# Kernel optimization log

Measured on AMD Instinct MI355X. Metric: run time of the kernel, lower is better.

The kernel has to match this reference:

```python
import jax, jax.numpy as jnp
import numpy as np

A = 1.0          # jacobi a
B = 1.0          # jacobi b
BASE_ALPHA = 2.0
K = 10           # polynomial order
N = 16384        # nodes
C = 32           # channels


def setup_inputs() -> dict:
    key = jax.random.key(0)
    k1, k2 = jax.random.split(key, 2)
    x = jax.random.normal(k1, (N, C), dtype=jnp.float32)
    # dense graph operator (stand-in for a normalized laplacian); scaled so spectrum is O(1)
    L = jax.random.normal(k2, (N, N), dtype=jnp.float32) / np.float32(np.sqrt(N))
    conv_params = jnp.full((K + 1,), min(1.0 / BASE_ALPHA, 1.0), dtype=jnp.float32)
    comb_params = jnp.ones((K + 1, C), dtype=jnp.float32)
    return {"x": x, "L": L, "conv_params": conv_params, "comb_params": comb_params}


def reference(x, L, conv_params, comb_params):
    a, b = A, B
    alpha = BASE_ALPHA * jnp.tanh(conv_params)  # [K+1] learned step sizes
    polys = [x]  # P_0 = x
    if K >= 1:
        # with l=-1, r=1: (r+l)/(r-l)=0, 1/(r-l)=0.5
        c1 = alpha[0] * (a - b) / 2.0
        c2 = alpha[0] * (a + b + 2.0) / 2.0
        polys.append(c1 * x + c2 * (L @ x))
    for i in range(2, K + 1):
        div = 2.0 * i * (i + a + b) * (2.0 * i + a + b - 2.0)
        r1 = (2.0 * i + a + b) * (2.0 * i + a + b - 1.0) * (2.0 * i + a + b - 2.0) / div
        r2 = (2.0 * i + a + b - 1.0) * (a * a - b * b) / div
        r3 = 2.0 * (i + a - 1.0) * (i + b - 1.0) * (2.0 * i + a + b) / div
        c1 = alpha[i - 1] * r1                      # multiplies L @ P_{i-1} (coef1, since 2/(r-l)=1)
        c2 = alpha[i - 1] * r2                      # coef2 (the (r+l)/(r-l) term vanishes)
        c3 = alpha[i - 1] * alpha[i - 2] * r3       # coef_3
        polys.append(c1 * (L @ polys[-1]) + c2 * polys[-1] - c3 * polys[-2])
    # y = sum_k comb[k] (broadcast over nodes) * P_k  -- avoids materializing the stacked [K+1,N,C]
    y = polys[0] * comb_params[0][None, :]
    for k in range(1, K + 1):
        y = y + comb_params[k][None, :] * polys[k]
    return y
```

## Files before the change

### kernel.cpp

```cpp
#include <hip/hip_runtime.h>
#include <math.h>


#define NN 16384
#define CC 32
#define KPOLY 10
#define NSPLIT 16
#define KSEG (NN / NSPLIT)
#define STEPS (KSEG / 32)
#define NTK (NN / 32)

typedef _Float16 half8 __attribute__((ext_vector_type(8)));
typedef float f32x4 __attribute__((ext_vector_type(4)));
typedef unsigned int u32x4 __attribute__((ext_vector_type(4)));
typedef unsigned int u32x2 __attribute__((ext_vector_type(2)));

union U16 {
  u32x4 u;
  half8 h;
};
union H4 {
  _Float16 h[4];
  u32x2 u;
};

__global__ __launch_bounds__(256) void conv_pack_gemm1(const float* __restrict__ L,
                                                       _Float16* __restrict__ Lf,
                                                       const _Float16* __restrict__ Ph,
                                                       float* __restrict__ part) {
  __shared__ __align__(16) _Float16 lds[16 * 1024];
  const int tid = threadIdx.x;
  const int tr = blockIdx.x >> 4;
  const int sc = blockIdx.x & 15;
  const float* src = L + (size_t)tr * 16 * NN + (size_t)sc * 1024;

#pragma unroll
  for (int j = 0; j < 16; ++j) {
    const int flat = j * 256 + tid;
    const int r = flat >> 8;
    const int cu = flat & 255;
    f32x4 v = __builtin_nontemporal_load(
        reinterpret_cast<const f32x4*>(src + (size_t)r * NN) + cu);
    H4 o;
    o.h[0] = (_Float16)v.x;
    o.h[1] = (_Float16)v.y;
    o.h[2] = (_Float16)v.z;
    o.h[3] = (_Float16)v.w;
    const int u = (cu >> 1) ^ (r & 7);
    *reinterpret_cast<u32x2*>(&lds[r * 1024 + u * 8 + (cu & 1) * 4]) = o.u;
  }
  __syncthreads();

  const int lane = tid & 63;
  const int wave = tid >> 6;
  const int r = lane & 15;
  const int lg = lane >> 4;

  f32x4 acc0 = (f32x4){0.f, 0.f, 0.f, 0.f};
  f32x4 acc1 = (f32x4){0.f, 0.f, 0.f, 0.f};
#pragma unroll
  for (int i = 0; i < 8; ++i) {
    const int tkl = wave * 8 + i;
    const int u = (tkl * 4 + lg) ^ (r & 7);
    U16 aval;
    aval.u = *reinterpret_cast<const u32x4*>(&lds[r * 1024 + u * 8]);
    const size_t tk = (size_t)sc * 32 + tkl;
    __builtin_nontemporal_store(
        aval.u, reinterpret_cast<u32x4*>(Lf + ((size_t)tr * NTK + tk) * 512) + lane);
    const int kb = sc * 128 + tkl * 4 + lg;
    U16 b0, b1;
    b0.u = *reinterpret_cast<const u32x4*>(Ph + (size_t)kb * 256 + (size_t)r * 8);
    b1.u = *reinterpret_cast<const u32x4*>(Ph + (size_t)kb * 256 + (size_t)(16 + r) * 8);
    acc0 = __builtin_amdgcn_mfma_f32_16x16x32_f16(aval.h, b0.h, acc0, 0, 0, 0);
    acc1 = __builtin_amdgcn_mfma_f32_16x16x32_f16(aval.h, b1.h, acc1, 0, 0, 0);
  }
  __syncthreads();

  float* red = reinterpret_cast<float*>(lds);
#pragma unroll
  for (int j = 0; j < 4; ++j) {
    red[wave * 512 + (lg * 4 + j) * 32 + r] = acc0[j];
    red[wave * 512 + (lg * 4 + j) * 32 + 16 + r] = acc1[j];
  }
  __syncthreads();

  const int e = tid * 2;
  float2 s0 = *reinterpret_cast<const float2*>(&red[e]);
  float2 s1 = *reinterpret_cast<const float2*>(&red[512 + e]);
  float2 s2 = *reinterpret_cast<const float2*>(&red[1024 + e]);
  float2 s3 = *reinterpret_cast<const float2*>(&red[1536 + e]);
  float2 s = make_float2(s0.x + s1.x + s2.x + s3.x, s0.y + s1.y + s2.y + s3.y);
  *reinterpret_cast<float2*>(part + (size_t)sc * NN * CC + (size_t)tr * 16 * CC + e) = s;
}

__global__ __launch_bounds__(256, 4) void gemm_f16(const _Float16* __restrict__ Lf,
                                                   const _Float16* __restrict__ Ph,
                                                   float* __restrict__ part) {
  const int tid = threadIdx.x;
  const int lane = tid & 63;
  const int wave = tid >> 6;
  const int rg = blockIdx.x & 63;
  const int split = blockIdx.x >> 6;
  const int rb = rg * 256 + wave * 64;
  const int k0 = split * KSEG;
  const int tk0 = k0 >> 5;
  const int l15 = lane & 15;
  const int lg = lane >> 4;

  const u32x4* Ap[4];
#pragma unroll
  for (int rt = 0; rt < 4; ++rt)
    Ap[rt] = reinterpret_cast<const u32x4*>(
                 Lf + ((size_t)((rb >> 4) + rt) * NTK + tk0) * 512) +
             lane;
  const u32x4* Bp[2];
#pragma unroll
  for (int ct = 0; ct < 2; ++ct)
    Bp[ct] = reinterpret_cast<const u32x4*>(Ph + (size_t)(k0 / 8 + lg) * 256 +
                                            (size_t)(ct * 16 + l15) * 8);

  f32x4 acc[4][2];
#pragma unroll
  for (int rt = 0; rt < 4; ++rt)
#pragma unroll
    for (int ct = 0; ct < 2; ++ct) acc[rt][ct] = (f32x4){0.f, 0.f, 0.f, 0.f};

  U16 A[2][4], B[2][2];
#pragma unroll
  for (int rt = 0; rt < 4; ++rt) A[0][rt].u = __builtin_nontemporal_load(Ap[rt]);
#pragma unroll
  for (int ct = 0; ct < 2; ++ct) B[0][ct].u = *Bp[ct];

#pragma unroll
  for (int kk = 0; kk < STEPS; ++kk) {
    const int cur = kk & 1;
    const int nxt = cur ^ 1;
    if (kk < STEPS - 1) {
#pragma unroll
      for (int rt = 0; rt < 4; ++rt)
        A[nxt][rt].u = __builtin_nontemporal_load(Ap[rt] + (kk + 1) * 64);
#pragma unroll
      for (int ct = 0; ct < 2; ++ct)
        B[nxt][ct].u = *reinterpret_cast<const u32x4*>(
            reinterpret_cast<const _Float16*>(Bp[ct]) + 1024 * (kk + 1));
    }
#pragma unroll
    for (int rt = 0; rt < 4; ++rt)
#pragma unroll
      for (int ct = 0; ct < 2; ++ct)
        acc[rt][ct] = __builtin_amdgcn_mfma_f32_16x16x32_f16(A[cur][rt].h, B[cur][ct].h,
                                                             acc[rt][ct], 0, 0, 0);
  }

  float* pb = part + (size_t)split * NN * CC;
#pragma unroll
  for (int rt = 0; rt < 4; ++rt)
#pragma unroll
    for (int ct = 0; ct < 2; ++ct)
#pragma unroll
      for (int j = 0; j < 4; ++j)
        pb[(size_t)(rb + rt * 16 + lg * 4 + j) * CC + ct * 16 + l15] = acc[rt][ct][j];
}

__global__ __launch_bounds__(256) void init_kernel(const float* __restrict__ x,
                                                   const float* __restrict__ comb,
                                                   float* __restrict__ y,
                                                   _Float16* __restrict__ Ph) {
  int idx = blockIdx.x * blockDim.x + threadIdx.x;
  float4 xv = reinterpret_cast<const float4*>(x)[idx];
  int c4 = (idx & 7) << 2;
  int n = idx >> 3;
  float4 cb = *reinterpret_cast<const float4*>(comb + c4);
  reinterpret_cast<float4*>(y)[idx] =
      make_float4(xv.x * cb.x, xv.y * cb.y, xv.z * cb.z, xv.w * cb.w);
  size_t pb = (size_t)(n >> 3) * 256 + (size_t)c4 * 8 + (n & 7);
  Ph[pb] = (_Float16)xv.x;
  Ph[pb + 8] = (_Float16)xv.y;
  Ph[pb + 16] = (_Float16)xv.z;
  Ph[pb + 24] = (_Float16)xv.w;
}

__global__ __launch_bounds__(256) void poly_update(
    const float* __restrict__ part, float* __restrict__ Pnew,
    const float* __restrict__ Pprev, const float* __restrict__ Pprev2,
    float* __restrict__ y, _Float16* __restrict__ Ph, const float* __restrict__ conv,
    const float* __restrict__ comb_row, float r1, float r2, float r3, int ia, int ib,
    int has2) {
  int idx = blockIdx.x * blockDim.x + threadIdx.x;
  float a1 = 2.f * tanhf(conv[ia]);
  float cL = a1 * r1;
  float cP = a1 * r2;

  float4 t = make_float4(0.f, 0.f, 0.f, 0.f);
#pragma unroll
  for (int s = 0; s < NSPLIT; ++s) {
    float4 p = reinterpret_cast<const float4*>(part)[(size_t)s * (NN * CC / 4) + idx];
    t.x += p.x;
    t.y += p.y;
    t.z += p.z;
    t.w += p.w;
  }

  float4 pp = reinterpret_cast<const float4*>(Pprev)[idx];
  float4 pn;
  pn.x = cL * t.x + cP * pp.x;
  pn.y = cL * t.y + cP * pp.y;
  pn.z = cL * t.z + cP * pp.z;
  pn.w = cL * t.w + cP * pp.w;
  if (has2) {
    float a2 = 2.f * tanhf(conv[ib]);
    float cPP = a1 * a2 * r3;
    float4 p2 = reinterpret_cast<const float4*>(Pprev2)[idx];
    pn.x -= cPP * p2.x;
    pn.y -= cPP * p2.y;
    pn.z -= cPP * p2.z;
    pn.w -= cPP * p2.w;
  }
  reinterpret_cast<float4*>(Pnew)[idx] = pn;

  int c4 = (idx & 7) << 2;
  int n = idx >> 3;
  size_t pb = (size_t)(n >> 3) * 256 + (size_t)c4 * 8 + (n & 7);
  Ph[pb] = (_Float16)pn.x;
  Ph[pb + 8] = (_Float16)pn.y;
  Ph[pb + 16] = (_Float16)pn.z;
  Ph[pb + 24] = (_Float16)pn.w;

  float4 cb = *reinterpret_cast<const float4*>(comb_row + c4);
  float4 yv = reinterpret_cast<float4*>(y)[idx];
  yv.x = fmaf(cb.x, pn.x, yv.x);
  yv.y = fmaf(cb.y, pn.y, yv.y);
  yv.z = fmaf(cb.z, pn.z, yv.z);
  yv.w = fmaf(cb.w, pn.w, yv.w);
  reinterpret_cast<float4*>(y)[idx] = yv;
}

static void jacobi_r(int i, double a, double b, float& r1, float& r2, float& r3) {
  double div = 2.0 * i * (i + a + b) * (2.0 * i + a + b - 2.0);
  r1 = (float)((2.0 * i + a + b) * (2.0 * i + a + b - 1.0) * (2.0 * i + a + b - 2.0) / div);
  r2 = (float)((2.0 * i + a + b - 1.0) * (a * a - b * b) / div);
  r3 = (float)(2.0 * (i + a - 1.0) * (i + b - 1.0) * (2.0 * i + a + b) / div);
}

extern "C" void kernel_launch(void* const* d_in, const int* in_sizes, int n_in,
                              void* d_out, int out_size, void* d_ws, size_t ws_size,
                              hipStream_t stream) {
  const float* x = (const float*)d_in[0];
  const float* Lm = (const float*)d_in[1];
  const float* conv = (const float*)d_in[2];
  const float* comb = (const float*)d_in[3];
  float* y = (float*)d_out;
  char* ws = (char*)d_ws;

  _Float16* Lf = (_Float16*)ws;
  float* part = (float*)(ws + 536870912ull);
  _Float16* Ph = (_Float16*)(ws + 536870912ull + 33554432ull);
  float* Pb0 = (float*)(ws + 536870912ull + 33554432ull + 2097152ull);
  float* Pb1 = Pb0 + (size_t)NN * CC;
  float* Pb2 = Pb1 + (size_t)NN * CC;
  float* bufs[3] = {Pb0, Pb1, Pb2};

  const double Aj = 1.0, Bj = 1.0;
  const int ew_blocks = NN * CC / 4 / 256;

  init_kernel<<<ew_blocks, 256, 0, stream>>>(x, comb, y, Ph);
  conv_pack_gemm1<<<16384, 256, 0, stream>>>(Lm, Lf, Ph, part);

  const float* Pprev = x;
  const float* Pprev2 = x;
  for (int i = 1; i <= KPOLY; ++i) {
    if (i > 1) gemm_f16<<<64 * NSPLIT, 256, 0, stream>>>(Lf, Ph, part);

    float r1, r2, r3;
    if (i == 1) {
      r1 = (float)((Aj + Bj + 2.0) / 2.0);
      r2 = (float)((Aj - Bj) / 2.0);
      r3 = 0.f;
    } else {
      jacobi_r(i, Aj, Bj, r1, r2, r3);
    }
    float* Pn = bufs[(i - 1) % 3];
    poly_update<<<ew_blocks, 256, 0, stream>>>(part, Pn, Pprev, Pprev2, y, Ph, conv,
                                               comb + (size_t)i * CC, r1, r2, r3, i - 1,
                                               (i >= 2) ? i - 2 : 0, (i >= 2) ? 1 : 0);
    Pprev2 = Pprev;
    Pprev = Pn;
  }
}
```

Before: 1.276 ms.

## Fuse split-K GEMM with polynomial update via in-block K reduction

Replaces the split-K GEMM (16 splits writing fp32 partials) plus a separate poly_update pass with a single kernel. Each block owns 16 rows, its four waves split K and reduce through LDS, and the recurrence update, fp16 repack and y accumulation are applied in the epilogue. The fp16 P buffer is double-buffered (ping-pong) so the next iteration's operand can be written while other blocks still read the current one. This removes the 32 MB partial write/read per iteration and one launch per step, but each wave now does only 2 MFMAs per A load across 1024 blocks, which changes occupancy and per-block work balance.

```diff
diff --git a/kernel.cpp b/kernel.cpp
--- a/kernel.cpp
+++ b/kernel.cpp
@@ -6,8 +6,6 @@
 #define CC 32
 #define KPOLY 10
 #define NSPLIT 16
-#define KSEG (NN / NSPLIT)
-#define STEPS (KSEG / 32)
 #define NTK (NN / 32)
 
 typedef _Float16 half8 __attribute__((ext_vector_type(8)));
@@ -93,73 +91,89 @@
   *reinterpret_cast<float2*>(part + (size_t)sc * NN * CC + (size_t)tr * 16 * CC + e) = s;
 }
 
-__global__ __launch_bounds__(256, 4) void gemm_f16(const _Float16* __restrict__ Lf,
-                                                   const _Float16* __restrict__ Ph,
-                                                   float* __restrict__ part) {
+__global__ __launch_bounds__(256, 4) void gemm_poly(
+    const _Float16* __restrict__ Lf, const _Float16* __restrict__ PhIn,
+    const float* __restrict__ Pprev, const float* __restrict__ Pprev2,
+    float* __restrict__ Pnew, _Float16* __restrict__ PhOut, float* __restrict__ y,
+    const float* __restrict__ conv, const float* __restrict__ comb_row, float r1,
+    float r2, float r3, int ia, int ib) {
   const int tid = threadIdx.x;
   const int lane = tid & 63;
   const int wave = tid >> 6;
-  const int rg = blockIdx.x & 63;
-  const int split = blockIdx.x >> 6;
-  const int rb = rg * 256 + wave * 64;
-  const int k0 = split * KSEG;
-  const int tk0 = k0 >> 5;
+  const int tr = blockIdx.x;
   const int l15 = lane & 15;
   const int lg = lane >> 4;
 
-  const u32x4* Ap[4];
-#pragma unroll
-  for (int rt = 0; rt < 4; ++rt)
-    Ap[rt] = reinterpret_cast<const u32x4*>(
-                 Lf + ((size_t)((rb >> 4) + rt) * NTK + tk0) * 512) +
-             lane;
-  const u32x4* Bp[2];
-#pragma unroll
-  for (int ct = 0; ct < 2; ++ct)
-    Bp[ct] = reinterpret_cast<const u32x4*>(Ph + (size_t)(k0 / 8 + lg) * 256 +
-                                            (size_t)(ct * 16 + l15) * 8);
-
-  f32x4 acc[4][2];
-#pragma unroll
-  for (int rt = 0; rt < 4; ++rt)
-#pragma unroll
-    for (int ct = 0; ct < 2; ++ct) acc[rt][ct] = (f32x4){0.f, 0.f, 0.f, 0.f};
-
-  U16 A[2][4], B[2][2];
-#pragma unroll
-  for (int rt = 0; rt < 4; ++rt) A[0][rt].u = __builtin_nontemporal_load(Ap[rt]);
-#pragma unroll
-  for (int ct = 0; ct < 2; ++ct) B[0][ct].u = *Bp[ct];
-
-#pragma unroll
-  for (int kk = 0; kk < STEPS; ++kk) {
-    const int cur = kk & 1;
-    const int nxt = cur ^ 1;
-    if (kk < STEPS - 1) {
-#pragma unroll
-      for (int rt = 0; rt < 4; ++rt)
-        A[nxt][rt].u = __builtin_nontemporal_load(Ap[rt] + (kk + 1) * 64);
-#pragma unroll
-      for (int ct = 0; ct < 2; ++ct)
-        B[nxt][ct].u = *reinterpret_cast<const u32x4*>(
-            reinterpret_cast<const _Float16*>(Bp[ct]) + 1024 * (kk + 1));
+  const int tk0 = wave * 128;
+  const u32x4* Ap =
+      reinterpret_cast<const u32x4*>(Lf + ((size_t)tr * NTK + tk0) * 512) + lane;
+  const _Float16* Bbase = PhIn + (size_t)(tk0 * 4 + lg) * 256 + (size_t)l15 * 8;
+
+  f32x4 acc0 = (f32x4){0.f, 0.f, 0.f, 0.f};
+  f32x4 acc1 = (f32x4){0.f, 0.f, 0.f, 0.f};
+
+  U16 A0, A1, B00, B01, B10, B11;
+  A0.u = __builtin_nontemporal_load(Ap);
+  B00.u = *reinterpret_cast<const u32x4*>(Bbase);
+  B01.u = *reinterpret_cast<const u32x4*>(Bbase + 128);
+
+  for (int kk = 0; kk < 128; kk += 2) {
+    A1.u = __builtin_nontemporal_load(Ap + (kk + 1) * 64);
+    B10.u = *reinterpret_cast<const u32x4*>(Bbase + (size_t)(kk + 1) * 1024);
+    B11.u = *reinterpret_cast<const u32x4*>(Bbase + (size_t)(kk + 1) * 1024 + 128);
+    acc0 = __builtin_amdgcn_mfma_f32_16x16x32_f16(A0.h, B00.h, acc0, 0, 0, 0);
+    acc1 = __builtin_amdgcn_mfma_f32_16x16x32_f16(A0.h, B01.h, acc1, 0, 0, 0);
+    if (kk + 2 < 128) {
+      A0.u = __builtin_nontemporal_load(Ap + (kk + 2) * 64);
+      B00.u = *reinterpret_cast<const u32x4*>(Bbase + (size_t)(kk + 2) * 1024);
+      B01.u = *reinterpret_cast<const u32x4*>(Bbase + (size_t)(kk + 2) * 1024 + 128);
     }
-#pragma unroll
-    for (int rt = 0; rt < 4; ++rt)
-#pragma unroll
-      for (int ct = 0; ct < 2; ++ct)
-        acc[rt][ct] = __builtin_amdgcn_mfma_f32_16x16x32_f16(A[cur][rt].h, B[cur][ct].h,
-                                                             acc[rt][ct], 0, 0, 0);
-  }
-
-  float* pb = part + (size_t)split * NN * CC;
-#pragma unroll
-  for (int rt = 0; rt < 4; ++rt)
-#pragma unroll
-    for (int ct = 0; ct < 2; ++ct)
-#pragma unroll
-      for (int j = 0; j < 4; ++j)
-        pb[(size_t)(rb + rt * 16 + lg * 4 + j) * CC + ct * 16 + l15] = acc[rt][ct][j];
+    acc0 = __builtin_amdgcn_mfma_f32_16x16x32_f16(A1.h, B10.h, acc0, 0, 0, 0);
+    acc1 = __builtin_amdgcn_mfma_f32_16x16x32_f16(A1.h, B11.h, acc1, 0, 0, 0);
+  }
+
+  __shared__ float red[4 * 512];
+#pragma unroll
+  for (int j = 0; j < 4; ++j) {
+    red[wave * 512 + (lg * 4 + j) * 32 + l15] = acc0[j];
+    red[wave * 512 + (lg * 4 + j) * 32 + 16 + l15] = acc1[j];
+  }
+  __syncthreads();
+
+  const int e = tid * 2;
+  float2 s0 = *reinterpret_cast<const float2*>(&red[e]);
+  float2 s1 = *reinterpret_cast<const float2*>(&red[512 + e]);
+  float2 s2 = *reinterpret_cast<const float2*>(&red[1024 + e]);
+  float2 s3 = *reinterpret_cast<const float2*>(&red[1536 + e]);
+  float2 t = make_float2(s0.x + s1.x + s2.x + s3.x, s0.y + s1.y + s2.y + s3.y);
+
+  const int row = e >> 5;
+  const int c = e & 31;
+  const int n = tr * 16 + row;
+  const size_t g = (size_t)n * CC + c;
+
+  const float a1 = 2.f * tanhf(conv[ia]);
+  const float a2 = 2.f * tanhf(conv[ib]);
+  const float cL = a1 * r1;
+  const float cP = a1 * r2;
+  const float cPP = a1 * a2 * r3;
+
+  float2 pp = *reinterpret_cast<const float2*>(Pprev + g);
+  float2 p2 = *reinterpret_cast<const float2*>(Pprev2 + g);
+  float2 pn;
+  pn.x = cL * t.x + cP * pp.x - cPP * p2.x;
+  pn.y = cL * t.y + cP * pp.y - cPP * p2.y;
+  *reinterpret_cast<float2*>(Pnew + g) = pn;
+
+  const size_t pb = (size_t)(n >> 3) * 256 + (size_t)c * 8 + (n & 7);
+  PhOut[pb] = (_Float16)pn.x;
+  PhOut[pb + 8] = (_Float16)pn.y;
+
+  float2 cb = *reinterpret_cast<const float2*>(comb_row + c);
+  float2 yv = *reinterpret_cast<float2*>(y + g);
+  yv.x = fmaf(cb.x, pn.x, yv.x);
+  yv.y = fmaf(cb.y, pn.y, yv.y);
+  *reinterpret_cast<float2*>(y + g) = yv;
 }
 
 __global__ __launch_bounds__(256) void init_kernel(const float* __restrict__ x,
@@ -182,10 +196,9 @@
 
 __global__ __launch_bounds__(256) void poly_update(
     const float* __restrict__ part, float* __restrict__ Pnew,
-    const float* __restrict__ Pprev, const float* __restrict__ Pprev2,
-    float* __restrict__ y, _Float16* __restrict__ Ph, const float* __restrict__ conv,
-    const float* __restrict__ comb_row, float r1, float r2, float r3, int ia, int ib,
-    int has2) {
+    const float* __restrict__ Pprev, float* __restrict__ y,
+    _Float16* __restrict__ PhOut, const float* __restrict__ conv,
+    const float* __restrict__ comb_row, float r1, float r2, int ia) {
   int idx = blockIdx.x * blockDim.x + threadIdx.x;
   float a1 = 2.f * tanhf(conv[ia]);
   float cL = a1 * r1;
@@ -207,24 +220,15 @@
   pn.y = cL * t.y + cP * pp.y;
   pn.z = cL * t.z + cP * pp.z;
   pn.w = cL * t.w + cP * pp.w;
-  if (has2) {
-    float a2 = 2.f * tanhf(conv[ib]);
-    float cPP = a1 * a2 * r3;
-    float4 p2 = reinterpret_cast<const float4*>(Pprev2)[idx];
-    pn.x -= cPP * p2.x;
-    pn.y -= cPP * p2.y;
-    pn.z -= cPP * p2.z;
-    pn.w -= cPP * p2.w;
-  }
   reinterpret_cast<float4*>(Pnew)[idx] = pn;
 
   int c4 = (idx & 7) << 2;
   int n = idx >> 3;
   size_t pb = (size_t)(n >> 3) * 256 + (size_t)c4 * 8 + (n & 7);
-  Ph[pb] = (_Float16)pn.x;
-  Ph[pb + 8] = (_Float16)pn.y;
-  Ph[pb + 16] = (_Float16)pn.z;
-  Ph[pb + 24] = (_Float16)pn.w;
+  PhOut[pb] = (_Float16)pn.x;
+  PhOut[pb + 8] = (_Float16)pn.y;
+  PhOut[pb + 16] = (_Float16)pn.z;
+  PhOut[pb + 24] = (_Float16)pn.w;
 
   float4 cb = *reinterpret_cast<const float4*>(comb_row + c4);
   float4 yv = reinterpret_cast<float4*>(y)[idx];
@@ -254,8 +258,9 @@
 
   _Float16* Lf = (_Float16*)ws;
   float* part = (float*)(ws + 536870912ull);
-  _Float16* Ph = (_Float16*)(ws + 536870912ull + 33554432ull);
-  float* Pb0 = (float*)(ws + 536870912ull + 33554432ull + 2097152ull);
+  _Float16* PhA = (_Float16*)(ws + 536870912ull + 33554432ull);
+  _Float16* PhB = PhA + (size_t)NN * CC;
+  float* Pb0 = (float*)(ws + 536870912ull + 33554432ull + 4194304ull);
   float* Pb1 = Pb0 + (size_t)NN * CC;
   float* Pb2 = Pb1 + (size_t)NN * CC;
   float* bufs[3] = {Pb0, Pb1, Pb2};
@@ -263,26 +268,27 @@
   const double Aj = 1.0, Bj = 1.0;
   const int ew_blocks = NN * CC / 4 / 256;
 
-  init_kernel<<<ew_blocks, 256, 0, stream>>>(x, comb, y, Ph);
-  conv_pack_gemm1<<<16384, 256, 0, stream>>>(Lm, Lf, Ph, part);
-
-  const float* Pprev = x;
+  init_kernel<<<ew_blocks, 256, 0, stream>>>(x, comb, y, PhA);
+  conv_pack_gemm1<<<16384, 256, 0, stream>>>(Lm, Lf, PhA, part);
+
+  {
+    float r1 = (float)((Aj + Bj + 2.0) / 2.0);
+    float r2 = (float)((Aj - Bj) / 2.0);
+    poly_update<<<ew_blocks, 256, 0, stream>>>(part, bufs[0], x, y, PhB, conv,
+                                               comb + CC, r1, r2, 0);
+  }
+
+  const float* Pprev = bufs[0];
   const float* Pprev2 = x;
-  for (int i = 1; i <= KPOLY; ++i) {
-    if (i > 1) gemm_f16<<<64 * NSPLIT, 256, 0, stream>>>(Lf, Ph, part);
-
+  for (int i = 2; i <= KPOLY; ++i) {
     float r1, r2, r3;
-    if (i == 1) {
-      r1 = (float)((Aj + Bj + 2.0) / 2.0);
-      r2 = (float)((Aj - Bj) / 2.0);
-      r3 = 0.f;
-    } else {
-      jacobi_r(i, Aj, Bj, r1, r2, r3);
-    }
+    jacobi_r(i, Aj, Bj, r1, r2, r3);
     float* Pn = bufs[(i - 1) % 3];
-    poly_update<<<ew_blocks, 256, 0, stream>>>(part, Pn, Pprev, Pprev2, y, Ph, conv,
-                                               comb + (size_t)i * CC, r1, r2, r3, i - 1,
-                                               (i >= 2) ? i - 2 : 0, (i >= 2) ? 1 : 0);
+    const _Float16* PhIn = (i & 1) ? PhA : PhB;
+    _Float16* PhOut = (i & 1) ? PhB : PhA;
+    gemm_poly<<<NN / 16, 256, 0, stream>>>(Lf, PhIn, Pprev, Pprev2, Pn, PhOut, y,
+                                           conv, comb + (size_t)i * CC, r1, r2, r3,
+                                           i - 1, i - 2);
     Pprev2 = Pprev;
     Pprev = Pn;
   }
```

Result: slower. 1.397 ms (+9.5%).
